# Performance work log

Hardware: AMD Instinct MI355X
Metric: run time of the kernel (lower is better)

Reference implementation:

```python
import jax, jax.numpy as jnp
import numpy as np

WS = 8          # window_size
NH = 8          # num_heads
DIM = 256
INNER = 256     # inner_dim (QK)
CINNER = 64     # coords_inner_dim
INNER_V = 256


def _rms(x, g, eps=1e-6):
    return x * jax.lax.rsqrt(jnp.mean(x * x, axis=-1, keepdims=True) + eps) * g


def _window(x, ws):
    # (b, H, W, d) -> (b, Wh, Ww, ws*ws, d)
    b, H, W, d = x.shape
    Wh, Ww = H // ws, W // ws
    x = x.reshape(b, Wh, ws, Ww, ws, d).transpose(0, 1, 3, 2, 4, 5)
    return x.reshape(b, Wh, Ww, ws * ws, d)


def _unwindow(x, Wh, Ww, ws):
    # (b, Wh*Ww, ws*ws, d) -> (b, Wh*ws, Ww*ws, d)
    b = x.shape[0]
    d = x.shape[-1]
    x = x.reshape(b, Wh, Ww, ws, ws, d).transpose(0, 1, 3, 2, 4, 5)
    return x.reshape(b, Wh * ws, Ww * ws, d)


def _embed_source(x, c, fqk_w, fqk_b, fqk_g, cqk_w, cqk_b, cqk_g, v_w):
    b = x.shape[0]
    xw = _window(x, WS)           # (b, Wh, Ww, n, dim)
    cw = _window(c, WS)
    Wh, Ww = xw.shape[1], xw.shape[2]
    f_avg = xw.mean(axis=3)       # (b, Wh, Ww, dim)
    c_avg = cw.mean(axis=3)
    f_qk = _rms(f_avg @ fqk_w.T + fqk_b, fqk_g).reshape(b, Wh * Ww, 2 * INNER)
    c_qk = _rms(c_avg @ cqk_w.T + cqk_b, cqk_g).reshape(b, Wh * Ww, 2 * CINNER)
    v = (xw @ v_w.T).reshape(b, Wh * Ww, WS * WS * INNER_V)
    return f_qk, c_qk, v, (Wh, Ww)


def setup_inputs() -> dict:
    key = jax.random.key(0)
    ks = jax.random.split(key, 8)
    s = 0.02
    return {
        "x1": jax.random.normal(ks[0], (4, 128, 128, DIM), jnp.float32),
        "c1": jax.random.normal(ks[1], (4, 128, 128, 4), jnp.float32),
        "x2": jax.random.normal(ks[2], (4, 96, 96, DIM), jnp.float32),
        "c2": jax.random.normal(ks[3], (4, 96, 96, 4), jnp.float32),
        "fqk_w": jax.random.normal(ks[4], (2 * INNER, DIM), jnp.float32) * s,
        "fqk_b": jnp.zeros((2 * INNER,), jnp.float32),
        "fqk_g": jnp.ones((2 * INNER,), jnp.float32),
        "cqk_w": jax.random.normal(ks[5], (2 * CINNER, 4), jnp.float32) * s,
        "cqk_b": jnp.zeros((2 * CINNER,), jnp.float32),
        "cqk_g": jnp.ones((2 * CINNER,), jnp.float32),
        "v_w": jax.random.normal(ks[6], (INNER_V, DIM), jnp.float32) * s,
        "vb_w": jax.random.normal(ks[7], (DIM, INNER_V), jnp.float32) * s,
    }


def reference(x1, c1, x2, c2, fqk_w, fqk_b, fqk_g, cqk_w, cqk_b, cqk_g, v_w, vb_w):
    b = x1.shape[0]
    f1, cc1, v1, (Wh1, Ww1) = _embed_source(x1, c1, fqk_w, fqk_b, fqk_g, cqk_w, cqk_b, cqk_g, v_w)
    f2, cc2, v2, (Wh2, Ww2) = _embed_source(x2, c2, fqk_w, fqk_b, fqk_g, cqk_w, cqk_b, cqk_g, v_w)
    n1, n2 = Wh1 * Ww1, Wh2 * Ww2
    N = n1 + n2

    f_qk = jnp.concatenate([f1, f2], axis=1)   # (b, N, 2*INNER)
    c_qk = jnp.concatenate([cc1, cc2], axis=1) # (b, N, 2*CINNER)
    values = jnp.concatenate([v1, v2], axis=1) # (b, N, WS*WS*INNER_V)

    f_q, f_k = jnp.split(f_qk, 2, axis=-1)
    c_q, c_k = jnp.split(c_qk, 2, axis=-1)

    dh = INNER // NH
    dch = CINNER // NH
    dv = values.shape[-1] // NH
    fq = f_q.reshape(b, N, NH, dh)
    fk = f_k.reshape(b, N, NH, dh)
    cq = c_q.reshape(b, N, NH, dch)
    ck = c_k.reshape(b, N, NH, dch)
    vh = values.reshape(b, N, NH, dv)

    scores = jnp.einsum("bnhd,bmhd->bhnm", fq, fk) / np.sqrt(dh)
    scores = scores + jnp.einsum("bnhd,bmhd->bhnm", cq, ck) / np.sqrt(dch)

    # mask self-attention within each source (block-diagonal masked out)
    seg = jnp.concatenate([jnp.zeros((n1,), jnp.int32), jnp.ones((n2,), jnp.int32)])
    allowed = seg[:, None] != seg[None, :]                     # (N, N) True = keep
    scores = jnp.where(allowed[None, None], scores, jnp.finfo(scores.dtype).min)

    attn = jax.nn.softmax(scores, axis=-1)                      # (b, h, N, N)
    v_out = jnp.einsum("bhnm,bmhd->bnhd", attn, vh).reshape(b, N, NH * dv)

    v_out = v_out.reshape(b, N, WS * WS, INNER_V)
    features_out = v_out @ vb_w.T                               # (b, N, ws*ws, dim)

    out1 = _unwindow(features_out[:, :n1], Wh1, Ww1, WS)
    out2 = _unwindow(features_out[:, n1:], Wh2, Ww2, WS)
    return out1, out2
```

## Files before the change

kernel.cpp:

```cpp
#include <hip/hip_runtime.h>
#include <hip/hip_bf16.h>

#define B 4
#define NH 8
#define N1 256
#define N2 144
#define NW 400
#define OUT2_OFF ((size_t)16777216)

typedef __attribute__((ext_vector_type(8))) short short8v;
typedef __attribute__((ext_vector_type(4))) float f32x4;
typedef __attribute__((ext_vector_type(2))) unsigned uint2v;
typedef __attribute__((ext_vector_type(4))) unsigned uint4v;

static __device__ __forceinline__ short f2bf(float f) {
    __hip_bfloat16 h = __float2bfloat16(f);
    return __builtin_bit_cast(short, h);
}

__global__ void prep_kernel(const float* __restrict__ v_w, const float* __restrict__ vb_w,
                            short* __restrict__ Mbf) {
    int d = blockIdx.x;
    int k = threadIdx.x;
    float s = 0.f;
    for (int j = 0; j < 256; ++j)
        s += vb_w[d * 256 + j] * v_w[j * 256 + k];
    size_t idx = ((((size_t)((d >> 4) * 8 + (k >> 5))) * 4 + ((k >> 3) & 3)) * 16 + (d & 15)) * 8 + (k & 7);
    Mbf[idx] = f2bf(s);
}

__global__ void transpose_fqk(const float* __restrict__ fqk_w, float* __restrict__ fqk_wT) {
    int o = blockIdx.x;
    int k = threadIdx.x;
    fqk_wT[(size_t)k * 512 + o] = fqk_w[(size_t)o * 256 + k];
}

__global__ void stage1_kernel(const float* __restrict__ x1, const float* __restrict__ c1,
                              const float* __restrict__ x2, const float* __restrict__ c2,
                              const float* __restrict__ fqk_wT, const float* __restrict__ fqk_b,
                              const float* __restrict__ fqk_g,
                              const float* __restrict__ cqk_w, const float* __restrict__ cqk_b,
                              const float* __restrict__ cqk_g,
                              short* __restrict__ qcat, short* __restrict__ kcat,
                              short* __restrict__ Xw3) {
    int blk = blockIdx.x;
    int b = blk / NW, n = blk % NW;
    int t = threadIdx.x;

    __shared__ float favg[256];
    __shared__ float cavg[4];
    __shared__ float red[256];

    const float* xbase;
    int rstride;
    if (n < N1) {
        xbase = x1 + (((size_t)b * 128 + (n >> 4) * 8) * 128 + (n & 15) * 8) * 256;
        rstride = 128 * 256;
    } else {
        int nn = n - N1;
        xbase = x2 + (((size_t)b * 96 + (nn / 12) * 8) * 96 + (nn % 12) * 8) * 256;
        rstride = 96 * 256;
    }

    int rt = b * 100 + (n >> 2);
    int RlocBase = (n & 3) * 64;
    short* xw_base = Xw3 + (((size_t)rt * 8 + (t >> 5)) * 256) * 32 + (t & 31);

    float acc = 0.f;
    #pragma unroll 4
    for (int p = 0; p < 64; ++p) {
        float v = xbase[(p >> 3) * rstride + (p & 7) * 256 + t];
        acc += v;
        xw_base[(RlocBase + p) * 32] = f2bf(v);
    }
    favg[t] = acc * (1.f / 64.f);

    if (t < 64) {
        const float* cbase;
        int crs;
        if (n < N1) {
            cbase = c1 + (((size_t)b * 128 + (n >> 4) * 8) * 128 + (n & 15) * 8) * 4;
            crs = 128 * 4;
        } else {
            int nn = n - N1;
            cbase = c2 + (((size_t)b * 96 + (nn / 12) * 8) * 96 + (nn % 12) * 8) * 4;
            crs = 96 * 4;
        }
        float4 v = *(const float4*)(cbase + (t >> 3) * crs + (t & 7) * 4);
        for (int off = 32; off > 0; off >>= 1) {
            v.x += __shfl_down(v.x, off, 64);
            v.y += __shfl_down(v.y, off, 64);
            v.z += __shfl_down(v.z, off, 64);
            v.w += __shfl_down(v.w, off, 64);
        }
        if (t == 0) {
            cavg[0] = v.x * (1.f / 64.f);
            cavg[1] = v.y * (1.f / 64.f);
            cavg[2] = v.z * (1.f / 64.f);
            cavg[3] = v.w * (1.f / 64.f);
        }
    }
    __syncthreads();

    float o1 = fqk_b[t], o2 = fqk_b[t + 256];
    for (int k = 0; k < 256; ++k) {
        float fa = favg[k];
        o1 += fa * fqk_wT[(size_t)k * 512 + t];
        o2 += fa * fqk_wT[(size_t)k * 512 + 256 + t];
    }
    red[t] = o1 * o1 + o2 * o2;
    __syncthreads();
    for (int s = 128; s > 0; s >>= 1) {
        if (t < s) red[t] += red[t + s];
        __syncthreads();
    }
    float scale = rsqrtf(red[0] / 512.f + 1e-6f);

    const float SF = 0.17677669529663687f;
    {
        int h = t >> 5, j = t & 31;
        size_t qb = ((size_t)(b * 8 + h) * NW + n) * 64;
        qcat[qb + j] = f2bf(o1 * scale * fqk_g[t] * SF);
        kcat[qb + j] = f2bf(o2 * scale * fqk_g[t + 256]);
    }
    __syncthreads();

    float co = 0.f;
    if (t < 128) {
        co = cqk_b[t];
        #pragma unroll
        for (int k = 0; k < 4; ++k) co += cavg[k] * cqk_w[t * 4 + k];
    }
    red[t] = (t < 128) ? co * co : 0.f;
    __syncthreads();
    for (int s = 128; s > 0; s >>= 1) {
        if (t < s) red[t] += red[t + s];
        __syncthreads();
    }
    float cscale = rsqrtf(red[0] / 128.f + 1e-6f);

    const float SC = 0.35355339059327373f;
    if (t < 64) {
        int h = t >> 3, j = 32 + (t & 7);
        qcat[((size_t)(b * 8 + h) * NW + n) * 64 + j] = f2bf(co * cscale * cqk_g[t] * SC);
    } else if (t < 128) {
        int tt = t - 64;
        int h = tt >> 3, j = 32 + (tt & 7);
        kcat[((size_t)(b * 8 + h) * NW + n) * 64 + j] = f2bf(co * cscale * cqk_g[t]);
    } else {
        int tt = t - 128;
        for (int z = tt; z < 384; z += 128) {
            int which = z & 1;
            int zz = z >> 1;
            int h = zz / 24, j = 40 + zz % 24;
            short* dst = which ? kcat : qcat;
            dst[((size_t)(b * 8 + h) * NW + n) * 64 + j] = 0;
        }
    }
}

template <int NMT>
static __device__ __forceinline__ void scores_wave(const short* __restrict__ qcat,
                                                   const short* __restrict__ kcat,
                                                   short* __restrict__ Pb,
                                                   int b, int h, int n0, int mbase, int lane) {
    int l15 = lane & 15, g = lane >> 4;
    int kl8 = g * 8;
    size_t rowb = (size_t)(b * 8 + h) * NW;

    const short* qrow = qcat + (rowb + n0 + l15) * 64;
    short8v bf0 = *(const short8v*)(qrow + kl8);
    short8v bf1 = *(const short8v*)(qrow + 32 + kl8);

    f32x4 acc[NMT];
    #pragma unroll
    for (int i = 0; i < NMT; ++i) acc[i] = (f32x4)0.f;

    #pragma unroll
    for (int mt = 0; mt < NMT; ++mt) {
        const short* krow = kcat + (rowb + mbase + mt * 16 + l15) * 64;
        short8v af0 = *(const short8v*)(krow + kl8);
        short8v af1 = *(const short8v*)(krow + 32 + kl8);
        acc[mt] = __builtin_amdgcn_mfma_f32_16x16x32_bf16(af0, bf0, acc[mt], 0, 0, 0);
        acc[mt] = __builtin_amdgcn_mfma_f32_16x16x32_bf16(af1, bf1, acc[mt], 0, 0, 0);
    }

    float mx = -3.4e38f;
    #pragma unroll
    for (int mt = 0; mt < NMT; ++mt)
        #pragma unroll
        for (int r = 0; r < 4; ++r) mx = fmaxf(mx, acc[mt][r]);
    mx = fmaxf(mx, __shfl_xor(mx, 16, 64));
    mx = fmaxf(mx, __shfl_xor(mx, 32, 64));

    float sum = 0.f;
    #pragma unroll
    for (int mt = 0; mt < NMT; ++mt)
        #pragma unroll
        for (int r = 0; r < 4; ++r) {
            float e = __expf(acc[mt][r] - mx);
            acc[mt][r] = e;
            sum += e;
        }
    sum += __shfl_xor(sum, 16, 64);
    sum += __shfl_xor(sum, 32, 64);
    float inv = 1.f / sum;

    int n = n0 + l15;
    short* prow = Pb + ((size_t)(b * 8 + h) * 512 + n) * 416;
    #pragma unroll
    for (int mt = 0; mt < NMT; ++mt) {
        int m = mbase + mt * 16 + g * 4;
        *(short4*)(prow + m) = make_short4(f2bf(acc[mt][0] * inv), f2bf(acc[mt][1] * inv),
                                           f2bf(acc[mt][2] * inv), f2bf(acc[mt][3] * inv));
    }
}

__global__ __launch_bounds__(256) void scores_kernel(const short* __restrict__ qcat,
                                                     const short* __restrict__ kcat,
                                                     short* __restrict__ Pb) {
    int wid = blockIdx.x * 4 + (threadIdx.x >> 6);
    int lane = threadIdx.x & 63;
    if (wid < 512) {
        int b = wid >> 7, h = (wid >> 4) & 7, n0 = (wid & 15) * 16;
        scores_wave<9>(qcat, kcat, Pb, b, h, n0, 256, lane);
    } else {
        int t3 = wid - 512;
        int b = t3 / 72, r = t3 % 72;
        int h = r / 9, n0 = 256 + (r % 9) * 16;
        scores_wave<16>(qcat, kcat, Pb, b, h, n0, 0, lane);
    }
}

__global__ __launch_bounds__(256, 2) void wproj_mfma(const short* __restrict__ Xw3,
                                                     const short* __restrict__ Mbf,
                                                     short* __restrict__ Wb) {
    int bid = blockIdx.x;
    int dt = bid & 1, rh = (bid >> 1) & 1, rt = bid >> 2;
    int tid = threadIdx.x;
    int lane = tid & 63, w = tid >> 6;
    int wd = w & 1, wrR = w >> 1;
    int l15 = lane & 15, g = lane >> 4;

    __shared__ short lds[2][128][40];

    int idx0 = tid, idx1 = tid + 256;
    int R0 = idx0 >> 2, c0 = idx0 & 3;
    int R1 = idx1 >> 2, c1 = idx1 & 3;

    short8v st0, st1;
    {
        const short* s = Xw3 + (((size_t)rt * 8 + 0) * 256 + rh * 128) * 32;
        st0 = *(const short8v*)(s + idx0 * 8);
        st1 = *(const short8v*)(s + idx1 * 8);
    }

    f32x4 acc[4][4] = {};
    for (int kc = 0; kc < 8; ++kc) {
        int buf = kc & 1;
        *(short8v*)&lds[buf][R0][c0 * 8] = st0;
        *(short8v*)&lds[buf][R1][c1 * 8] = st1;
        if (kc < 7) {
            const short* s = Xw3 + (((size_t)rt * 8 + kc + 1) * 256 + rh * 128) * 32;
            st0 = *(const short8v*)(s + idx0 * 8);
            st1 = *(const short8v*)(s + idx1 * 8);
        }
        short8v af[4];
        #pragma unroll
        for (int mi = 0; mi < 4; ++mi) {
            int dtile = dt * 8 + wd * 4 + mi;
            af[mi] = *(const short8v*)(Mbf + ((size_t)(dtile * 8 + kc)) * 512 + lane * 8);
        }
        __syncthreads();
        #pragma unroll
        for (int ni = 0; ni < 4; ++ni) {
            int Rl = wrR * 64 + ni * 16 + l15;
            short8v bf = *(const short8v*)&lds[buf][Rl][g * 8];
            #pragma unroll
            for (int mi = 0; mi < 4; ++mi)
                acc[mi][ni] = __builtin_amdgcn_mfma_f32_16x16x32_bf16(af[mi], bf, acc[mi][ni], 0, 0, 0);
        }
    }

    int dq = dt * 128 + wd * 64 + g * 4;
    #pragma unroll
    for (int ni = 0; ni < 4; ++ni) {
        size_t Rg = (size_t)rt * 256 + rh * 128 + wrR * 64 + ni * 16 + l15;
        short* wp = Wb + Rg * 256 + dq;
        #pragma unroll
        for (int mi = 0; mi < 4; ++mi) {
            f32x4 a = acc[mi][ni];
            *(short4*)(wp + mi * 16) = make_short4(f2bf(a[0]), f2bf(a[1]), f2bf(a[2]), f2bf(a[3]));
        }
    }
}

__global__ __launch_bounds__(256, 2) void pv_mfma(
    const short* __restrict__ Pb, const short* __restrict__ Wb,
    float* __restrict__ out) {
    int bid = blockIdx.x;
    int dt = bid & 1;
    int nt = (bid >> 1) & 3;
    int p  = (bid >> 3) & 63;
    int b  = bid >> 9;
    int h  = p >> 3;
    int tid = threadIdx.x;
    int lane = tid & 63;
    int w = tid >> 6;
    int wr = w >> 1;
    int wc = w & 1;
    int l15 = lane & 15;
    int kl8 = (lane >> 4) << 3;

    __shared__ short8v Bs[512];
    unsigned ldsBase = (unsigned)(size_t)&Bs[0];

    int n0 = nt * 128;
    int mlo = (nt < 2) ? 256 : 0;
    int mhi = (nt < 2) ? 400 : 256;
    int d0 = dt * 128;

    const short* arow[4];
    #pragma unroll
    for (int mi = 0; mi < 4; ++mi) {
        int n = n0 + wr * 64 + mi * 16 + l15;
        arow[mi] = Pb + ((size_t)(b * 8 + h) * 512 + n) * 416 + kl8;
    }

    f32x4 acc[4][4] = {};

    int mrow0 = tid >> 4;
    int doff0 = (tid & 15) << 3;
    int mrow1 = (tid + 256) >> 4;
    int doff1 = doff0;

    const size_t wbBase = ((size_t)b * 400) * 64 * 256 + (size_t)p * 256 + d0;

    short8v cur0, cur1;
    {
        int gm0 = mlo + mrow0, gm1 = mlo + mrow1;
        cur0 = (gm0 < mhi) ? *(const short8v*)(Wb + wbBase + (size_t)gm0 * 64 * 256 + doff0) : (short8v)0;
        cur1 = (gm1 < mhi) ? *(const short8v*)(Wb + wbBase + (size_t)gm1 * 64 * 256 + doff1) : (short8v)0;
    }

    for (int m0 = mlo; m0 < mhi; m0 += 32) {
        short8v af[4];
        #pragma unroll
        for (int mi = 0; mi < 4; ++mi)
            af[mi] = *(const short8v*)(arow[mi] + m0);

        __syncthreads();
        {
            int par = (mrow0 >> 2) & 1, gg = mrow0 >> 3, r = mrow0 & 3;
            int nb = doff0 >> 4, c0h = (doff0 >> 3) & 1;
            Bs[(par * 8 + nb) * 32 + gg * 8 + r * 2 + c0h] = cur0;
            par = (mrow1 >> 2) & 1; gg = mrow1 >> 3; r = mrow1 & 3;
            nb = doff1 >> 4; c0h = (doff1 >> 3) & 1;
            Bs[(par * 8 + nb) * 32 + gg * 8 + r * 2 + c0h] = cur1;
        }
        if (m0 + 32 < mhi) {
            int gm0 = m0 + 32 + mrow0, gm1 = m0 + 32 + mrow1;
            cur0 = (gm0 < mhi) ? *(const short8v*)(Wb + wbBase + (size_t)gm0 * 64 * 256 + doff0) : (short8v)0;
            cur1 = (gm1 < mhi) ? *(const short8v*)(Wb + wbBase + (size_t)gm1 * 64 * 256 + doff1) : (short8v)0;
        }
        __syncthreads();

        short8v bf[4];
        #pragma unroll
        for (int ni = 0; ni < 4; ++ni) {
            int nb = wc * 4 + ni;
            unsigned a0 = ldsBase + (unsigned)((0 * 8 + nb) * 512 + lane * 8);
            unsigned a1 = ldsBase + (unsigned)((1 * 8 + nb) * 512 + lane * 8);
            uint2v lo, hi;
            asm volatile("ds_read_b64_tr_b16 %0, %1" : "=v"(lo) : "v"(a0));
            asm volatile("ds_read_b64_tr_b16 %0, %1" : "=v"(hi) : "v"(a1));
            uint4v bw; bw.x = lo.x; bw.y = lo.y; bw.z = hi.x; bw.w = hi.y;
            bf[ni] = __builtin_bit_cast(short8v, bw);
        }
        asm volatile("s_waitcnt lgkmcnt(0)" ::: "memory");
        __builtin_amdgcn_sched_barrier(0);

        #pragma unroll
        for (int mi = 0; mi < 4; ++mi) {
            #pragma unroll
            for (int ni = 0; ni < 4; ++ni)
                acc[mi][ni] = __builtin_amdgcn_mfma_f32_16x16x32_bf16(af[mi], bf[ni], acc[mi][ni], 0, 0, 0);
        }
    }

    int pr = p >> 3, pc = p & 7;
    #pragma unroll
    for (int mi = 0; mi < 4; ++mi) {
        #pragma unroll
        for (int r = 0; r < 4; ++r) {
            int n = n0 + wr * 64 + mi * 16 + ((lane >> 4) << 2) + r;
            if (n >= NW) continue;
            float* obase;
            if (n < N1) {
                obase = out + (((size_t)b * 128 + (n >> 4) * 8 + pr) * 128 + ((n & 15) << 3) + pc) * 256;
            } else {
                int nn = n - N1;
                obase = out + OUT2_OFF + (((size_t)b * 96 + (nn / 12) * 8 + pr) * 96 + (nn % 12) * 8 + pc) * 256;
            }
            #pragma unroll
            for (int ni = 0; ni < 4; ++ni)
                obase[d0 + wc * 64 + ni * 16 + l15] = acc[mi][ni][r];
        }
    }
}

extern "C" void kernel_launch(void* const* d_in, const int* in_sizes, int n_in,
                              void* d_out, int out_size, void* d_ws, size_t ws_size,
                              hipStream_t stream) {
    const float* x1    = (const float*)d_in[0];
    const float* c1    = (const float*)d_in[1];
    const float* x2    = (const float*)d_in[2];
    const float* c2    = (const float*)d_in[3];
    const float* fqk_w = (const float*)d_in[4];
    const float* fqk_b = (const float*)d_in[5];
    const float* fqk_g = (const float*)d_in[6];
    const float* cqk_w = (const float*)d_in[7];
    const float* cqk_b = (const float*)d_in[8];
    const float* cqk_g = (const float*)d_in[9];
    const float* v_w   = (const float*)d_in[10];
    const float* vb_w  = (const float*)d_in[11];
    float* out = (float*)d_out;

    char* wsb = (char*)d_ws;
    short* Mbf    = (short*)(wsb);
    float* fqk_wT = (float*)(wsb + 131072);
    short* qcat   = (short*)(wsb + 655360);
    short* kcat   = (short*)(wsb + 2293760);
    short* Pb     = (short*)(wsb + 3932160);
    short* Xw3    = (short*)(wsb + 17563648);
    short* Wb     = (short*)(wsb + 69992448);

    prep_kernel<<<256, 256, 0, stream>>>(v_w, vb_w, Mbf);
    transpose_fqk<<<512, 256, 0, stream>>>(fqk_w, fqk_wT);
    stage1_kernel<<<B * NW, 256, 0, stream>>>(x1, c1, x2, c2, fqk_wT, fqk_b, fqk_g,
                                              cqk_w, cqk_b, cqk_g, qcat, kcat, Xw3);
    wproj_mfma<<<1600, 256, 0, stream>>>(Xw3, Mbf, Wb);
    scores_kernel<<<200, 256, 0, stream>>>(qcat, kcat, Pb);
    pv_mfma<<<2048, 256, 0, stream>>>(Pb, Wb, out);
}
```

Before: 353.1 us.

## Drop bf16 Xw3 staging; read fp32 x directly in wproj and MFMA QK projection

Stage1 no longer writes a bf16 windowed copy of x. wproj_mfma now loads fp32 x directly from the original layout and converts it to bf16 in registers before the LDS stores, which removes a large intermediate write plus re-read. The per-window fp32 scalar QK projection is replaced by a separate MFMA kernel over bf16 averaged features and bf16 weights. This adds a kernel launch and lowers the precision of the QK projection to bf16, while wproj now issues strided fp32 gathers that cost twice the bytes of bf16 reads.

```diff
diff --git a/kernel.cpp b/kernel.cpp
--- a/kernel.cpp
+++ b/kernel.cpp
@@ -16,6 +16,14 @@
 static __device__ __forceinline__ short f2bf(float f) {
     __hip_bfloat16 h = __float2bfloat16(f);
     return __builtin_bit_cast(short, h);
+}
+
+static __device__ __forceinline__ const float* xrow_ptr(const float* x1, const float* x2,
+                                                        int b, int n, int p) {
+    if (n < N1)
+        return x1 + (((size_t)b * 128 + (n >> 4) * 8 + (p >> 3)) * 128 + (n & 15) * 8 + (p & 7)) * 256;
+    int nn = n - N1;
+    return x2 + (((size_t)b * 96 + (nn / 12) * 8 + (p >> 3)) * 96 + (nn % 12) * 8 + (p & 7)) * 256;
 }
 
 __global__ void prep_kernel(const float* __restrict__ v_w, const float* __restrict__ vb_w,
@@ -29,25 +37,21 @@
     Mbf[idx] = f2bf(s);
 }
 
-__global__ void transpose_fqk(const float* __restrict__ fqk_w, float* __restrict__ fqk_wT) {
-    int o = blockIdx.x;
-    int k = threadIdx.x;
-    fqk_wT[(size_t)k * 512 + o] = fqk_w[(size_t)o * 256 + k];
-}
-
-__global__ void stage1_kernel(const float* __restrict__ x1, const float* __restrict__ c1,
-                              const float* __restrict__ x2, const float* __restrict__ c2,
-                              const float* __restrict__ fqk_wT, const float* __restrict__ fqk_b,
-                              const float* __restrict__ fqk_g,
-                              const float* __restrict__ cqk_w, const float* __restrict__ cqk_b,
-                              const float* __restrict__ cqk_g,
-                              short* __restrict__ qcat, short* __restrict__ kcat,
-                              short* __restrict__ Xw3) {
+__global__ void wconv_kernel(const float* __restrict__ fqk_w, short* __restrict__ fqk_wb) {
+    int i = blockIdx.x * 256 + threadIdx.x;
+    fqk_wb[i] = f2bf(fqk_w[i]);
+}
+
+__global__ void mean_kernel(const float* __restrict__ x1, const float* __restrict__ c1,
+                            const float* __restrict__ x2, const float* __restrict__ c2,
+                            const float* __restrict__ cqk_w, const float* __restrict__ cqk_b,
+                            const float* __restrict__ cqk_g,
+                            short* __restrict__ favgb,
+                            short* __restrict__ qcat, short* __restrict__ kcat) {
     int blk = blockIdx.x;
     int b = blk / NW, n = blk % NW;
     int t = threadIdx.x;
 
-    __shared__ float favg[256];
     __shared__ float cavg[4];
     __shared__ float red[256];
 
@@ -62,18 +66,16 @@
         rstride = 96 * 256;
     }
 
-    int rt = b * 100 + (n >> 2);
-    int RlocBase = (n & 3) * 64;
-    short* xw_base = Xw3 + (((size_t)rt * 8 + (t >> 5)) * 256) * 32 + (t & 31);
-
-    float acc = 0.f;
-    #pragma unroll 4
-    for (int p = 0; p < 64; ++p) {
-        float v = xbase[(p >> 3) * rstride + (p & 7) * 256 + t];
-        acc += v;
-        xw_base[(RlocBase + p) * 32] = f2bf(v);
-    }
-    favg[t] = acc * (1.f / 64.f);
+    float a0 = 0.f, a1 = 0.f, a2 = 0.f, a3 = 0.f;
+    #pragma unroll
+    for (int pr = 0; pr < 8; ++pr) {
+        const float* rowp = xbase + (size_t)pr * rstride + t;
+        a0 += rowp[0 * 256] + rowp[4 * 256];
+        a1 += rowp[1 * 256] + rowp[5 * 256];
+        a2 += rowp[2 * 256] + rowp[6 * 256];
+        a3 += rowp[3 * 256] + rowp[7 * 256];
+    }
+    favgb[(size_t)blk * 256 + t] = f2bf((a0 + a1 + a2 + a3) * (1.f / 64.f));
 
     if (t < 64) {
         const float* cbase;
@@ -99,29 +101,6 @@
             cavg[2] = v.z * (1.f / 64.f);
             cavg[3] = v.w * (1.f / 64.f);
         }
-    }
-    __syncthreads();
-
-    float o1 = fqk_b[t], o2 = fqk_b[t + 256];
-    for (int k = 0; k < 256; ++k) {
-        float fa = favg[k];
-        o1 += fa * fqk_wT[(size_t)k * 512 + t];
-        o2 += fa * fqk_wT[(size_t)k * 512 + 256 + t];
-    }
-    red[t] = o1 * o1 + o2 * o2;
-    __syncthreads();
-    for (int s = 128; s > 0; s >>= 1) {
-        if (t < s) red[t] += red[t + s];
-        __syncthreads();
-    }
-    float scale = rsqrtf(red[0] / 512.f + 1e-6f);
-
-    const float SF = 0.17677669529663687f;
-    {
-        int h = t >> 5, j = t & 31;
-        size_t qb = ((size_t)(b * 8 + h) * NW + n) * 64;
-        qcat[qb + j] = f2bf(o1 * scale * fqk_g[t] * SF);
-        kcat[qb + j] = f2bf(o2 * scale * fqk_g[t + 256]);
     }
     __syncthreads();
 
@@ -159,6 +138,71 @@
     }
 }
 
+__global__ __launch_bounds__(256) void qkproj_kernel(const short* __restrict__ fqk_wb,
+                                                     const float* __restrict__ fqk_b,
+                                                     const float* __restrict__ fqk_g,
+                                                     const short* __restrict__ favgb,
+                                                     short* __restrict__ qcat,
+                                                     short* __restrict__ kcat) {
+    int w = threadIdx.x >> 6, lane = threadIdx.x & 63;
+    int ngl = w >> 1, half = w & 1;
+    int ngrp = blockIdx.x * 2 + ngl;
+    int l15 = lane & 15, g = lane >> 4;
+
+    __shared__ float ssb[2][2][16];
+
+    const short* frow = favgb + ((size_t)ngrp * 16 + l15) * 256;
+    short8v bf[8];
+    #pragma unroll
+    for (int c = 0; c < 8; ++c) bf[c] = *(const short8v*)(frow + c * 32 + g * 8);
+
+    f32x4 acc[16];
+    #pragma unroll
+    for (int i = 0; i < 16; ++i) acc[i] = (f32x4)0.f;
+
+    #pragma unroll
+    for (int mt = 0; mt < 16; ++mt) {
+        const short* arow = fqk_wb + ((size_t)(half * 256 + mt * 16 + l15)) * 256;
+        #pragma unroll
+        for (int c = 0; c < 8; ++c) {
+            short8v af = *(const short8v*)(arow + c * 32 + g * 8);
+            acc[mt] = __builtin_amdgcn_mfma_f32_16x16x32_bf16(af, bf[c], acc[mt], 0, 0, 0);
+        }
+    }
+
+    float ss = 0.f;
+    #pragma unroll
+    for (int mt = 0; mt < 16; ++mt) {
+        float4 bi = *(const float4*)(fqk_b + half * 256 + mt * 16 + g * 4);
+        acc[mt][0] += bi.x; acc[mt][1] += bi.y; acc[mt][2] += bi.z; acc[mt][3] += bi.w;
+        ss += acc[mt][0] * acc[mt][0] + acc[mt][1] * acc[mt][1]
+            + acc[mt][2] * acc[mt][2] + acc[mt][3] * acc[mt][3];
+    }
+    ss += __shfl_xor(ss, 16, 64);
+    ss += __shfl_xor(ss, 32, 64);
+    if (lane < 16) ssb[ngl][half][lane] = ss;
+    __syncthreads();
+    float scale = rsqrtf((ssb[ngl][0][l15] + ssb[ngl][1][l15]) / 512.f + 1e-6f);
+
+    int idx = ngrp * 16 + l15;
+    int b = idx / NW, n = idx % NW;
+    const float SF = 0.17677669529663687f;
+    float mult = half ? 1.f : SF;
+    short* dst = half ? kcat : qcat;
+
+    #pragma unroll
+    for (int mt = 0; mt < 16; ++mt) {
+        int ol = mt * 16 + g * 4;
+        float4 gg = *(const float4*)(fqk_g + half * 256 + ol);
+        int h = ol >> 5, j = ol & 31;
+        short4 s4 = make_short4(f2bf(acc[mt][0] * scale * gg.x * mult),
+                                f2bf(acc[mt][1] * scale * gg.y * mult),
+                                f2bf(acc[mt][2] * scale * gg.z * mult),
+                                f2bf(acc[mt][3] * scale * gg.w * mult));
+        *(short4*)(dst + ((size_t)(b * 8 + h) * NW + n) * 64 + j) = s4;
+    }
+}
+
 template <int NMT>
 static __device__ __forceinline__ void scores_wave(const short* __restrict__ qcat,
                                                    const short* __restrict__ kcat,
@@ -232,7 +276,8 @@
     }
 }
 
-__global__ __launch_bounds__(256, 2) void wproj_mfma(const short* __restrict__ Xw3,
+__global__ __launch_bounds__(256, 2) void wproj_mfma(const float* __restrict__ x1,
+                                                     const float* __restrict__ x2,
                                                      const short* __restrict__ Mbf,
                                                      short* __restrict__ Wb) {
     int bid = blockIdx.x;
@@ -244,26 +289,34 @@
 
     __shared__ short lds[2][128][40];
 
-    int idx0 = tid, idx1 = tid + 256;
-    int R0 = idx0 >> 2, c0 = idx0 & 3;
-    int R1 = idx1 >> 2, c1 = idx1 & 3;
-
-    short8v st0, st1;
-    {
-        const short* s = Xw3 + (((size_t)rt * 8 + 0) * 256 + rh * 128) * 32;
-        st0 = *(const short8v*)(s + idx0 * 8);
-        st1 = *(const short8v*)(s + idx1 * 8);
-    }
+    int b = rt / 100;
+    int nb0 = (rt % 100) * 4 + rh * 2;
+
+    int Rl0 = tid >> 2, oc = tid & 3;
+    int Rl1 = Rl0 + 64;
+    const float* src0 = xrow_ptr(x1, x2, b, nb0 + (Rl0 >> 6), Rl0 & 63) + oc * 8;
+    const float* src1 = xrow_ptr(x1, x2, b, nb0 + (Rl1 >> 6), Rl1 & 63) + oc * 8;
+
+    float4 p00 = *(const float4*)(src0);
+    float4 p01 = *(const float4*)(src0 + 4);
+    float4 p10 = *(const float4*)(src1);
+    float4 p11 = *(const float4*)(src1 + 4);
 
     f32x4 acc[4][4] = {};
     for (int kc = 0; kc < 8; ++kc) {
         int buf = kc & 1;
-        *(short8v*)&lds[buf][R0][c0 * 8] = st0;
-        *(short8v*)&lds[buf][R1][c1 * 8] = st1;
+        short8v s0, s1;
+        s0[0] = f2bf(p00.x); s0[1] = f2bf(p00.y); s0[2] = f2bf(p00.z); s0[3] = f2bf(p00.w);
+        s0[4] = f2bf(p01.x); s0[5] = f2bf(p01.y); s0[6] = f2bf(p01.z); s0[7] = f2bf(p01.w);
+        s1[0] = f2bf(p10.x); s1[1] = f2bf(p10.y); s1[2] = f2bf(p10.z); s1[3] = f2bf(p10.w);
+        s1[4] = f2bf(p11.x); s1[5] = f2bf(p11.y); s1[6] = f2bf(p11.z); s1[7] = f2bf(p11.w);
+        *(short8v*)&lds[buf][Rl0][oc * 8] = s0;
+        *(short8v*)&lds[buf][Rl1][oc * 8] = s1;
         if (kc < 7) {
-            const short* s = Xw3 + (((size_t)rt * 8 + kc + 1) * 256 + rh * 128) * 32;
-            st0 = *(const short8v*)(s + idx0 * 8);
-            st1 = *(const short8v*)(s + idx1 * 8);
+            const float* q0 = src0 + (kc + 1) * 32;
+            const float* q1 = src1 + (kc + 1) * 32;
+            p00 = *(const float4*)q0; p01 = *(const float4*)(q0 + 4);
+            p10 = *(const float4*)q1; p11 = *(const float4*)(q1 + 4);
         }
         short8v af[4];
         #pragma unroll
@@ -275,10 +328,10 @@
         #pragma unroll
         for (int ni = 0; ni < 4; ++ni) {
             int Rl = wrR * 64 + ni * 16 + l15;
-            short8v bf = *(const short8v*)&lds[buf][Rl][g * 8];
+            short8v bfv = *(const short8v*)&lds[buf][Rl][g * 8];
             #pragma unroll
             for (int mi = 0; mi < 4; ++mi)
-                acc[mi][ni] = __builtin_amdgcn_mfma_f32_16x16x32_bf16(af[mi], bf, acc[mi][ni], 0, 0, 0);
+                acc[mi][ni] = __builtin_amdgcn_mfma_f32_16x16x32_bf16(af[mi], bfv, acc[mi][ni], 0, 0, 0);
         }
     }
 
@@ -365,7 +418,7 @@
         }
         __syncthreads();
 
-        short8v bf[4];
+        short8v bfv[4];
         #pragma unroll
         for (int ni = 0; ni < 4; ++ni) {
             int nb = wc * 4 + ni;
@@ -375,7 +428,7 @@
             asm volatile("ds_read_b64_tr_b16 %0, %1" : "=v"(lo) : "v"(a0));
             asm volatile("ds_read_b64_tr_b16 %0, %1" : "=v"(hi) : "v"(a1));
             uint4v bw; bw.x = lo.x; bw.y = lo.y; bw.z = hi.x; bw.w = hi.y;
-            bf[ni] = __builtin_bit_cast(short8v, bw);
+            bfv[ni] = __builtin_bit_cast(short8v, bw);
         }
         asm volatile("s_waitcnt lgkmcnt(0)" ::: "memory");
         __builtin_amdgcn_sched_barrier(0);
@@ -384,7 +437,7 @@
         for (int mi = 0; mi < 4; ++mi) {
             #pragma unroll
             for (int ni = 0; ni < 4; ++ni)
-                acc[mi][ni] = __builtin_amdgcn_mfma_f32_16x16x32_bf16(af[mi], bf[ni], acc[mi][ni], 0, 0, 0);
+                acc[mi][ni] = __builtin_amdgcn_mfma_f32_16x16x32_bf16(af[mi], bfv[ni], acc[mi][ni], 0, 0, 0);
         }
     }
 
@@ -428,18 +481,19 @@
 
     char* wsb = (char*)d_ws;
     short* Mbf    = (short*)(wsb);
-    float* fqk_wT = (float*)(wsb + 131072);
-    short* qcat   = (short*)(wsb + 655360);
-    short* kcat   = (short*)(wsb + 2293760);
-    short* Pb     = (short*)(wsb + 3932160);
-    short* Xw3    = (short*)(wsb + 17563648);
-    short* Wb     = (short*)(wsb + 69992448);
+    short* fqk_wb = (short*)(wsb + 131072);
+    short* favgb  = (short*)(wsb + 393216);
+    short* qcat   = (short*)(wsb + 1212416);
+    short* kcat   = (short*)(wsb + 2850816);
+    short* Pb     = (short*)(wsb + 4489216);
+    short* Wb     = (short*)(wsb + 18120704);
 
     prep_kernel<<<256, 256, 0, stream>>>(v_w, vb_w, Mbf);
-    transpose_fqk<<<512, 256, 0, stream>>>(fqk_w, fqk_wT);
-    stage1_kernel<<<B * NW, 256, 0, stream>>>(x1, c1, x2, c2, fqk_wT, fqk_b, fqk_g,
-                                              cqk_w, cqk_b, cqk_g, qcat, kcat, Xw3);
-    wproj_mfma<<<1600, 256, 0, stream>>>(Xw3, Mbf, Wb);
+    wconv_kernel<<<512, 256, 0, stream>>>(fqk_w, fqk_wb);
+    mean_kernel<<<B * NW, 256, 0, stream>>>(x1, c1, x2, c2, cqk_w, cqk_b, cqk_g,
+                                            favgb, qcat, kcat);
+    qkproj_kernel<<<50, 256, 0, stream>>>(fqk_wb, fqk_b, fqk_g, favgb, qcat, kcat);
+    wproj_mfma<<<1600, 256, 0, stream>>>(x1, x2, Mbf, Wb);
     scores_kernel<<<200, 256, 0, stream>>>(qcat, kcat, Pb);
     pv_mfma<<<2048, 256, 0, stream>>>(Pb, Wb, out);
 }
```

Measured after the change: 343.2 us. 2.8% less time.
